# Optimization experiments

Measured on AMD Instinct MI355X. Metric: run time of the kernel, lower is better.

## Reference

```python
import jax, jax.numpy as jnp
import numpy as np

B, T, D, U = 32, 2048, 512, 512


def setup_inputs() -> dict:
    key = jax.random.key(0)
    ks = jax.random.split(key, 6)
    value = jax.random.normal(ks[0], (B, T, D), dtype=jnp.float32)
    query = jax.random.normal(ks[1], (B, D), dtype=jnp.float32)
    mask = jax.random.randint(ks[2], (B, T), 0, 2, dtype=jnp.int32)
    # Glorot-ish scaled dense weights (no bias, matching Dense(use_bias=False))
    W1 = jax.random.normal(ks[3], (D, U), dtype=jnp.float32) * (1.0 / np.sqrt(D))
    W2 = jax.random.normal(ks[4], (D, U), dtype=jnp.float32) * (1.0 / np.sqrt(D))
    V = jax.random.normal(ks[5], (U,), dtype=jnp.float32) * (1.0 / np.sqrt(U))
    return {"value": value, "query": query, "mask": mask, "W1": W1, "W2": W2, "V": V}


def reference(value, query, mask, W1, W2, V):
    # Additive (Bahdanau) attention scores: u[b,t] = V . tanh(value[b,t] @ W1 + query[b] @ W2)
    w1_key = jnp.einsum('btd,du->btu', value, W1)          # [B, T, U]
    w2_query = jnp.einsum('bd,du->bu', query, W2)          # [B, U]
    u = jnp.einsum('btu,u->bt', jnp.tanh(w1_key + w2_query[:, None, :]), V)  # [B, T]
    # Masking: add -1e20 where mask == 0 (same as keras reference)
    u = u + (1.0 - mask.astype(u.dtype)) * jnp.asarray(-1e20, dtype=u.dtype)
    a = jax.nn.softmax(u, axis=1)                          # [B, T]
    # Pointer extraction: gather value row at argmax of attention weights
    idx = jnp.argmax(a, axis=1)                            # [B]
    context = jnp.take_along_axis(value, idx[:, None, None], axis=1)[:, 0, :]  # [B, D]
    return (context, a)
```

## Files before the change

kernel.cpp:

```cpp
#include <hip/hip_runtime.h>
#include <hip/hip_fp16.h>
#include <stdint.h>

#define B_ 32
#define T_ 2048
#define D_ 512
#define U_ 512
#define M_ (B_ * T_)
#define MAXC 4
#define BK 32

typedef _Float16 half8   __attribute__((ext_vector_type(8)));
typedef float   floatx4  __attribute__((ext_vector_type(4)));

__device__ __forceinline__ float tanh_fast(float x) {
    float ax = fabsf(x);
    float e  = __expf(2.0f * ax);
    float t  = 1.0f - 2.0f / (e + 1.0f);
    return copysignf(t, x);
}

__device__ __forceinline__ void gld_lds16(const void* gsrc, void* lds_dst) {
    typedef __attribute__((address_space(1))) const char gch;
    typedef __attribute__((address_space(3))) char lch;
    __builtin_amdgcn_global_load_lds((const gch*)(uintptr_t)gsrc,
                                     (lch*)(uint32_t)(uintptr_t)lds_dst,
                                     16, 0, 0);
}

__global__ __launch_bounds__(256)
void k_prep(const float* __restrict__ W1, const float* __restrict__ query,
            const float* __restrict__ W2, _Float16* __restrict__ W1T,
            float* __restrict__ w2q) {
    const int bid = blockIdx.x;
    const int tid = threadIdx.x;
    if (bid < 64) {
        __shared__ float tile[64][65];
        const int bx = bid & 7, by = bid >> 3;
        const int k0 = bx * 64, n0 = by * 64;
        const int tx = tid & 63, ty = tid >> 6;
#pragma unroll
        for (int i = 0; i < 16; ++i) {
            int r = ty * 16 + i;
            tile[r][tx] = W1[(size_t)(k0 + r) * U_ + n0 + tx];
        }
        __syncthreads();
#pragma unroll
        for (int i = 0; i < 16; ++i) {
            int r = ty * 16 + i;
            W1T[(size_t)(n0 + r) * D_ + k0 + tx] = (_Float16)tile[tx][r];
        }
    } else {
        __shared__ float sq[D_];
        __shared__ float part[128];
        const int id = bid - 64;
        const int b  = id >> 2;
        const int nq = id & 3;
        sq[tid]       = query[b * D_ + tid];
        sq[tid + 256] = query[b * D_ + tid + 256];
        __syncthreads();
        const int n  = nq * 128 + (tid & 127);
        const int dh = tid >> 7;
        float acc = 0.f;
        const int d0 = dh * 256;
#pragma unroll 16
        for (int d = d0; d < d0 + 256; ++d)
            acc = fmaf(sq[d], W2[(size_t)d * U_ + n], acc);
        if (dh == 1) part[tid & 127] = acc;
        __syncthreads();
        if (dh == 0) w2q[b * U_ + n] = acc + part[tid];
    }
}

__global__ __launch_bounds__(1024, 4)
void k_gemm_u(const float* __restrict__ value,
              const _Float16* __restrict__ W1T,
              const float* __restrict__ w2q,
              const float* __restrict__ Vv,
              float* __restrict__ u_out) {
    __shared__ __align__(16) float    sA[2][128 * 32];
    __shared__ __align__(16) _Float16 sB[2][512 * 32];
    __shared__ float sRed[16][64];

    const int tid  = threadIdx.x;
    const int wv   = tid >> 6;
    const int l    = tid & 63;
    const int l15  = l & 15;
    const int lg   = l >> 4;
    const int m0   = blockIdx.x * 128;
    const int b    = m0 >> 11;
    const int wr   = (wv >> 3) * 64;
    const int wc   = (wv & 7) * 64;

    const int a_row = tid >> 3;
    const int a_lu  = (l & 7) ^ (l >> 3);
    const float* a_src = value + (size_t)(m0 + a_row) * D_ + a_lu * 4;
    const int b_lu = (l & 3) ^ ((l >> 3) & 3);
    const int b_n0 = (l >> 2);

#define ISSUE(c, buf)                                                          \
    {                                                                          \
        gld_lds16(a_src + (c) * BK, (void*)(&sA[buf][wv * 256]));              \
        _Pragma("unroll")                                                      \
        for (int j = 0; j < 2; ++j) {                                          \
            const int inst = wv * 2 + j;                                       \
            const int n = inst * 16 + b_n0;                                    \
            gld_lds16(W1T + (size_t)n * D_ + (c) * BK + b_lu * 8,              \
                      (void*)(&sB[buf][inst * 512]));                          \
        }                                                                      \
    }

    ISSUE(0, 0);

    floatx4 acc[4][4];
    const floatx4 zero4 = {0.f, 0.f, 0.f, 0.f};
#pragma unroll
    for (int i = 0; i < 4; ++i)
#pragma unroll
        for (int j = 0; j < 4; ++j) acc[i][j] = zero4;

    __syncthreads();

    for (int c = 0; c < 16; ++c) {
        const int cur = c & 1;
        if (c < 15) ISSUE(c + 1, cur ^ 1);

        half8 af[4];
#pragma unroll
        for (int mi = 0; mi < 4; ++mi) {
            const int row = wr + mi * 16 + l15;
            const int r7  = l15 & 7;
            const int p0  = (lg * 2) ^ r7;
            const int p1  = (lg * 2 + 1) ^ r7;
            const floatx4 x0 = *(const floatx4*)(&sA[cur][row * 32 + p0 * 4]);
            const floatx4 x1 = *(const floatx4*)(&sA[cur][row * 32 + p1 * 4]);
            half8 h;
#pragma unroll
            for (int q = 0; q < 4; ++q) {
                h[q]     = (_Float16)x0[q];
                h[4 + q] = (_Float16)x1[q];
            }
            af[mi] = h;
        }
        half8 bf[4];
#pragma unroll
        for (int ni = 0; ni < 4; ++ni) {
            const int n = wc + ni * 16 + l15;
            const int p = lg ^ ((l15 >> 1) & 3);
            bf[ni] = *(const half8*)(&sB[cur][n * 32 + p * 8]);
        }
#pragma unroll
        for (int ni = 0; ni < 4; ++ni)
#pragma unroll
            for (int mi = 0; mi < 4; ++mi)
                acc[mi][ni] = __builtin_amdgcn_mfma_f32_16x16x32_f16(
                    af[mi], bf[ni], acc[mi][ni], 0, 0, 0);
        __syncthreads();
    }
#undef ISSUE

    float ps[4][4];
#pragma unroll
    for (int mi = 0; mi < 4; ++mi)
#pragma unroll
        for (int j = 0; j < 4; ++j) ps[mi][j] = 0.f;
#pragma unroll
    for (int ni = 0; ni < 4; ++ni) {
        const int n = wc + ni * 16 + l15;
        const float w2 = w2q[b * U_ + n];
        const float vv = Vv[n];
#pragma unroll
        for (int mi = 0; mi < 4; ++mi)
#pragma unroll
            for (int j = 0; j < 4; ++j)
                ps[mi][j] += vv * tanh_fast(acc[mi][ni][j] + w2);
    }
#pragma unroll
    for (int off = 1; off < 16; off <<= 1)
#pragma unroll
        for (int mi = 0; mi < 4; ++mi)
#pragma unroll
            for (int j = 0; j < 4; ++j)
                ps[mi][j] += __shfl_xor(ps[mi][j], off, 64);

    if (l15 == 0) {
#pragma unroll
        for (int mi = 0; mi < 4; ++mi)
#pragma unroll
            for (int j = 0; j < 4; ++j)
                sRed[wv][mi * 16 + lg * 4 + j] = ps[mi][j];
    }
    __syncthreads();
    if (tid < 128) {
        const int half = tid >> 6, lr = tid & 63;
        float s = 0.f;
#pragma unroll
        for (int cw = 0; cw < 8; ++cw) s += sRed[half * 8 + cw][lr];
        u_out[m0 + tid] = s;
    }
}

__global__ __launch_bounds__(256)
void k_post(const float* __restrict__ u, const int* __restrict__ mask,
            float* __restrict__ a_out, int* __restrict__ cand_t,
            float* __restrict__ cand_score) {
    __shared__ float sx[T_];
    __shared__ float rv[4];
    __shared__ int   ri[4];
    __shared__ float s_scalar;

    const int b = blockIdx.x;
    const int tid = threadIdx.x;
    const int wave = tid >> 6, lane = tid & 63;

    if (tid < MAXC) cand_score[b * MAXC + tid] = 0.f;

#pragma unroll
    for (int i = 0; i < 8; ++i) {
        const int t = tid * 8 + i;
        float x = u[b * T_ + t];
        if (mask[b * T_ + t] == 0) x = -1e20f;
        sx[t] = x;
    }
    __syncthreads();

    for (int r = 0; r < MAXC; ++r) {
        float v = -INFINITY; int vi = 0;
#pragma unroll
        for (int i = 0; i < 8; ++i) {
            const int t = tid * 8 + i;
            const float x = sx[t];
            if (x > v) { v = x; vi = t; }
        }
        for (int off = 32; off > 0; off >>= 1) {
            const float ov = __shfl_down(v, off, 64);
            const int   oi = __shfl_down(vi, off, 64);
            if (ov > v || (ov == v && oi < vi)) { v = ov; vi = oi; }
        }
        if (lane == 0) { rv[wave] = v; ri[wave] = vi; }
        __syncthreads();
        if (tid == 0) {
            float bv = rv[0]; int bi = ri[0];
            for (int w = 1; w < 4; ++w)
                if (rv[w] > bv || (rv[w] == bv && ri[w] < bi)) { bv = rv[w]; bi = ri[w]; }
            cand_t[b * MAXC + r] = bi;
            if (r == 0) s_scalar = bv;
            sx[bi] = -INFINITY;
        }
        __syncthreads();
    }
    const float mx = s_scalar;

    float zloc = 0.f;
    float evals[8];
#pragma unroll
    for (int i = 0; i < 8; ++i) {
        const int t = tid * 8 + i;
        float x = u[b * T_ + t];
        if (mask[b * T_ + t] == 0) x = -1e20f;
        const float e = __expf(x - mx);
        evals[i] = e;
        zloc += e;
    }
    for (int off = 32; off > 0; off >>= 1) zloc += __shfl_down(zloc, off, 64);
    if (lane == 0) rv[wave] = zloc;
    __syncthreads();
    if (tid == 0) s_scalar = 1.0f / (rv[0] + rv[1] + rv[2] + rv[3]);
    __syncthreads();
    const float rz = s_scalar;
#pragma unroll
    for (int i = 0; i < 8; ++i) {
        const int t = tid * 8 + i;
        a_out[b * T_ + t] = evals[i] * rz;
    }
}

__global__ __launch_bounds__(256)
void k_resc(const float* __restrict__ value, const float* __restrict__ W1,
            const float* __restrict__ w2q, const float* __restrict__ Vv,
            const int* __restrict__ cand_t, float* __restrict__ cand_score) {
    __shared__ __align__(16) float vrows[MAXC][D_];
    __shared__ float part[4][MAXC][64];
    const int b  = blockIdx.x >> 3;
    const int nc = blockIdx.x & 7;
    const int tid = threadIdx.x;

#pragma unroll
    for (int ci = 0; ci < MAXC; ++ci) {
        const int t = cand_t[b * MAXC + ci];
        vrows[ci][tid]       = value[((size_t)b * T_ + t) * D_ + tid];
        vrows[ci][tid + 256] = value[((size_t)b * T_ + t) * D_ + tid + 256];
    }
    __syncthreads();

    const int q  = tid >> 6;
    const int nl = tid & 63;
    const int n  = nc * 64 + nl;
    float dq[MAXC] = {0.f, 0.f, 0.f, 0.f};
    const int d0 = q * 128;
#pragma unroll 8
    for (int d = d0; d < d0 + 128; ++d) {
        const float w = W1[(size_t)d * U_ + n];
#pragma unroll
        for (int ci = 0; ci < MAXC; ++ci)
            dq[ci] = fmaf(vrows[ci][d], w, dq[ci]);
    }
#pragma unroll
    for (int ci = 0; ci < MAXC; ++ci) part[q][ci][nl] = dq[ci];
    __syncthreads();

    if (q == 0) {
        const float w2 = w2q[b * U_ + n];
        const float vv = Vv[n];
        float sc[MAXC];
#pragma unroll
        for (int ci = 0; ci < MAXC; ++ci) {
            const float dot = part[0][ci][nl] + part[1][ci][nl]
                            + part[2][ci][nl] + part[3][ci][nl];
            sc[ci] = vv * tanhf(dot + w2);
        }
#pragma unroll
        for (int off = 1; off < 64; off <<= 1)
#pragma unroll
            for (int ci = 0; ci < MAXC; ++ci)
                sc[ci] += __shfl_xor(sc[ci], off, 64);
        if (nl == 0) {
#pragma unroll
            for (int ci = 0; ci < MAXC; ++ci)
                atomicAdd(&cand_score[b * MAXC + ci], sc[ci]);
        }
    }
}

__global__ __launch_bounds__(256)
void k_fin(const float* __restrict__ value, const int* __restrict__ mask,
           const int* __restrict__ cand_t, const float* __restrict__ cand_score,
           float* __restrict__ ctx_out) {
    __shared__ int s_t;
    const int b = blockIdx.x;
    const int tid = threadIdx.x;
    if (tid == 0) {
        float bv = -INFINITY; int bt = cand_t[b * MAXC];
        for (int i = 0; i < MAXC; ++i) {
            const int   t = cand_t[b * MAXC + i];
            float s = cand_score[b * MAXC + i];
            if (mask[b * T_ + t] == 0) s = -1e20f;
            if (s > bv || (s == bv && t < bt)) { bv = s; bt = t; }
        }
        s_t = bt;
    }
    __syncthreads();
    const int t = s_t;
    ctx_out[b * D_ + tid]       = value[((size_t)b * T_ + t) * D_ + tid];
    ctx_out[b * D_ + tid + 256] = value[((size_t)b * T_ + t) * D_ + tid + 256];
}

extern "C" void kernel_launch(void* const* d_in, const int* in_sizes, int n_in,
                              void* d_out, int out_size, void* d_ws, size_t ws_size,
                              hipStream_t stream) {
    const float* value = (const float*)d_in[0];
    const float* query = (const float*)d_in[1];
    const int*   mask  = (const int*)d_in[2];
    const float* W1    = (const float*)d_in[3];
    const float* W2    = (const float*)d_in[4];
    const float* Vv    = (const float*)d_in[5];

    char* ws = (char*)d_ws;
    _Float16* W1T        = (_Float16*)ws;
    float*    w2q        = (float*)(ws + 524288);
    float*    u_ws       = (float*)(ws + 589824);
    int*      cand_t     = (int*)(ws + 851968);
    float*    cand_score = (float*)(ws + 852480);

    float* ctx_out = (float*)d_out;
    float* a_out   = (float*)d_out + B_ * D_;

    hipLaunchKernelGGL(k_prep,   dim3(192), dim3(256), 0, stream,
                       W1, query, W2, W1T, w2q);
    hipLaunchKernelGGL(k_gemm_u, dim3(M_ / 128), dim3(1024), 0, stream,
                       value, W1T, w2q, Vv, u_ws);
    hipLaunchKernelGGL(k_post,   dim3(32), dim3(256), 0, stream,
                       u_ws, mask, a_out, cand_t, cand_score);
    hipLaunchKernelGGL(k_resc,   dim3(256), dim3(256), 0, stream,
                       value, W1, w2q, Vv, cand_t, cand_score);
    hipLaunchKernelGGL(k_fin,    dim3(32), dim3(256), 0, stream,
                       value, mask, cand_t, cand_score, ctx_out);
}
```

Baseline: 270.0 us.

## Convert A tile to fp16 once via registers and store fragment-ordered LDS layouts

The A (value) tile is now loaded into registers by half the threads, converted to fp16 once, and written to LDS in MFMA-fragment order. Previously every wave re-read fp32 data from LDS and converted it redundantly. B is also stored in fragment order so each lane does a single contiguous half8 read, with no swizzle. This cuts LDS footprint, LDS read traffic and conversion ALU work. In exchange, the A prefetch becomes register-staged rather than direct-to-LDS, which adds register pressure and may expose global load latency.

```diff
diff --git a/kernel.cpp b/kernel.cpp
--- a/kernel.cpp
+++ b/kernel.cpp
@@ -78,8 +78,8 @@
               const float* __restrict__ w2q,
               const float* __restrict__ Vv,
               float* __restrict__ u_out) {
-    __shared__ __align__(16) float    sA[2][128 * 32];
-    __shared__ __align__(16) _Float16 sB[2][512 * 32];
+    __shared__ __align__(16) _Float16 sA[2][512 * 8];
+    __shared__ __align__(16) _Float16 sB[2][2048 * 8];
     __shared__ float sRed[16][64];
 
     const int tid  = threadIdx.x;
@@ -92,25 +92,39 @@
     const int wr   = (wv >> 3) * 64;
     const int wc   = (wv & 7) * 64;
 
-    const int a_row = tid >> 3;
-    const int a_lu  = (l & 7) ^ (l >> 3);
-    const float* a_src = value + (size_t)(m0 + a_row) * D_ + a_lu * 4;
-    const int b_lu = (l & 3) ^ ((l >> 3) & 3);
-    const int b_n0 = (l >> 2);
-
-#define ISSUE(c, buf)                                                          \
+    const int mis  = tid >> 6;
+    const int lgs  = (tid >> 4) & 3;
+    const int l15s = tid & 15;
+    const float* a_src = value + (size_t)(m0 + mis * 16 + l15s) * D_ + lgs * 8;
+    const bool a_thread = (tid < 512);
+
+    const int b_n0 = l15;
+    const int b_k8 = lg * 8;
+
+#define B_ISSUE(c, buf)                                                        \
     {                                                                          \
-        gld_lds16(a_src + (c) * BK, (void*)(&sA[buf][wv * 256]));              \
         _Pragma("unroll")                                                      \
         for (int j = 0; j < 2; ++j) {                                          \
             const int inst = wv * 2 + j;                                       \
             const int n = inst * 16 + b_n0;                                    \
-            gld_lds16(W1T + (size_t)n * D_ + (c) * BK + b_lu * 8,              \
+            gld_lds16(W1T + (size_t)n * D_ + (c) * BK + b_k8,                  \
                       (void*)(&sB[buf][inst * 512]));                          \
         }                                                                      \
     }
 
-    ISSUE(0, 0);
+    B_ISSUE(0, 0);
+    floatx4 ra0, ra1;
+    if (a_thread) {
+        ra0 = *(const floatx4*)(a_src);
+        ra1 = *(const floatx4*)(a_src + 4);
+        half8 h;
+#pragma unroll
+        for (int q = 0; q < 4; ++q) {
+            h[q]     = (_Float16)ra0[q];
+            h[4 + q] = (_Float16)ra1[q];
+        }
+        *(half8*)(&sA[0][tid * 8]) = h;
+    }
 
     floatx4 acc[4][4];
     const floatx4 zero4 = {0.f, 0.f, 0.f, 0.f};
@@ -123,31 +137,24 @@
 
     for (int c = 0; c < 16; ++c) {
         const int cur = c & 1;
-        if (c < 15) ISSUE(c + 1, cur ^ 1);
-
-        half8 af[4];
+        if (c < 15) {
+            if (a_thread) {
+                ra0 = *(const floatx4*)(a_src + (c + 1) * BK);
+                ra1 = *(const floatx4*)(a_src + (c + 1) * BK + 4);
+            }
+            B_ISSUE(c + 1, cur ^ 1);
+        }
+
+        half8 af[4], bf[4];
 #pragma unroll
         for (int mi = 0; mi < 4; ++mi) {
-            const int row = wr + mi * 16 + l15;
-            const int r7  = l15 & 7;
-            const int p0  = (lg * 2) ^ r7;
-            const int p1  = (lg * 2 + 1) ^ r7;
-            const floatx4 x0 = *(const floatx4*)(&sA[cur][row * 32 + p0 * 4]);
-            const floatx4 x1 = *(const floatx4*)(&sA[cur][row * 32 + p1 * 4]);
-            half8 h;
-#pragma unroll
-            for (int q = 0; q < 4; ++q) {
-                h[q]     = (_Float16)x0[q];
-                h[4 + q] = (_Float16)x1[q];
-            }
-            af[mi] = h;
-        }
-        half8 bf[4];
+            const int mu = (wr >> 4) + mi;
+            af[mi] = *(const half8*)(&sA[cur][(mu * 64 + l) * 8]);
+        }
 #pragma unroll
         for (int ni = 0; ni < 4; ++ni) {
-            const int n = wc + ni * 16 + l15;
-            const int p = lg ^ ((l15 >> 1) & 3);
-            bf[ni] = *(const half8*)(&sB[cur][n * 32 + p * 8]);
+            const int inst = (wv & 7) * 4 + ni;
+            bf[ni] = *(const half8*)(&sB[cur][(inst * 64 + l) * 8]);
         }
 #pragma unroll
         for (int ni = 0; ni < 4; ++ni)
@@ -155,9 +162,19 @@
             for (int mi = 0; mi < 4; ++mi)
                 acc[mi][ni] = __builtin_amdgcn_mfma_f32_16x16x32_f16(
                     af[mi], bf[ni], acc[mi][ni], 0, 0, 0);
-        __syncthreads();
-    }
-#undef ISSUE
+
+        if (c < 15 && a_thread) {
+            half8 h;
+#pragma unroll
+            for (int q = 0; q < 4; ++q) {
+                h[q]     = (_Float16)ra0[q];
+                h[4 + q] = (_Float16)ra1[q];
+            }
+            *(half8*)(&sA[cur ^ 1][tid * 8]) = h;
+        }
+        __syncthreads();
+    }
+#undef B_ISSUE
 
     float ps[4][4];
 #pragma unroll
```

Result: no change. 271.2 us (+0.4%).
